# Performance work log

Hardware: AMD Instinct MI355X
Metric: run time of the kernel (lower is better)

Reference implementation:

```python
import jax, jax.numpy as jnp
import numpy as np

T, B, S, D, L, V = 32, 64, 64, 1024, 2, 32000


def _lstm_layer(x, h0, c0, wih, whh, bih, bhh):
    # x: (T, B, D_in); pytorch gate order: i, f, g, o
    b = bih + bhh
    xg = jnp.einsum('tbd,gd->tbg', x, wih) + b  # (T, B, 4D) precomputed input gates

    def step(carry, xg_t):
        h, c = carry
        gates = xg_t + h @ whh.T
        i, f, g, o = jnp.split(gates, 4, axis=-1)
        i, f, o = jax.nn.sigmoid(i), jax.nn.sigmoid(f), jax.nn.sigmoid(o)
        c = f * c + i * jnp.tanh(g)
        h = o * jnp.tanh(c)
        return (h, c), h

    (hT, cT), ys = jax.lax.scan(step, (h0, c0), xg)
    return ys, hT, cT


def setup_inputs() -> dict:
    key = jax.random.key(0)
    ks = jax.random.split(key, 20)
    s = 1.0 / np.sqrt(D)
    inp = {
        'input': jax.random.randint(ks[0], (T, B), 0, V),
        'h0': jax.random.normal(ks[1], (L, B, D)) * 0.1,
        'c0': jax.random.normal(ks[2], (L, B, D)) * 0.1,
        'context': jax.random.normal(ks[3], (S, B, D)) * 0.1,
        'init_output': jax.random.normal(ks[4], (B, D)) * 0.1,
        'emb_table': jax.random.normal(ks[5], (V, D)) * 0.02,
        'wih0': jax.random.normal(ks[6], (4 * D, D)) * s,
        'whh0': jax.random.normal(ks[7], (4 * D, D)) * s,
        'bih0': jax.random.normal(ks[8], (4 * D,)) * s,
        'bhh0': jax.random.normal(ks[9], (4 * D,)) * s,
        'wih1': jax.random.normal(ks[10], (4 * D, D)) * s,
        'whh1': jax.random.normal(ks[11], (4 * D, D)) * s,
        'bih1': jax.random.normal(ks[12], (4 * D,)) * s,
        'bhh1': jax.random.normal(ks[13], (4 * D,)) * s,
        'w_in': jax.random.normal(ks[14], (D, D)) * s,
        'w_out': jax.random.normal(ks[15], (D, 2 * D)) * s,
    }
    return inp


def reference(input, h0, c0, context, init_output, emb_table,
              wih0, whh0, bih0, bhh0, wih1, whh1, bih1, bhh1,
              w_in, w_out):
    # padding_idx=0 -> embedding row 0 is zero
    emb_table = emb_table.at[0].set(0.0)
    x = emb_table[input]  # (T, B, D)  (dropout=0 -> identity)

    layer_params = [(wih0, whh0, bih0, bhh0), (wih1, whh1, bih1, bhh1)]
    hs, cs = [], []
    for l in range(L):
        x, hT, cT = _lstm_layer(x, h0[l], c0[l], *layer_params[l])
        hs.append(hT)
        cs.append(cT)
    hn = jnp.stack(hs)  # (L, B, D)
    cn = jnp.stack(cs)

    # GlobalAttention over all timesteps at once (attn output never feeds back)
    ctx = jnp.transpose(context, (1, 0, 2))           # (B, S, D) == context.t()
    q = jnp.einsum('tbd,ed->tbe', x, w_in)            # linear_in(query)
    scores = jnp.einsum('tbd,bsd->tbs', q, ctx)       # (T, B, S)
    attn = jax.nn.softmax(scores, axis=-1)
    weighted = jnp.einsum('tbs,bsd->tbd', attn, ctx)  # (T, B, D)
    cat = jnp.concatenate([weighted, x], axis=-1)     # (T, B, 2D)
    out = jnp.tanh(jnp.einsum('tbe,de->tbd', cat, w_out))  # (T, B, D)

    return out, (hn, cn), attn[-1]
```

## Files before the change

### kernel.cpp

```cpp
#include <hip/hip_runtime.h>
#include <math.h>

#define T_ 32
#define B_ 64
#define S_ 64
#define D_ 1024

typedef __attribute__((ext_vector_type(8))) short short8;
typedef __attribute__((ext_vector_type(4))) float floatx4;

__device__ inline short8 ld8s(const short* p){ return *(const short8*)p; }
__device__ inline floatx4 mfma16(short8 a, short8 b, floatx4 c){
  return __builtin_amdgcn_mfma_f32_16x16x32_bf16(a, b, c, 0, 0, 0);
}
__device__ inline float sigm(float x){ return 1.0f/(1.0f+__expf(-x)); }

__device__ inline void load_lds16(const short* g, short* l){
  __builtin_amdgcn_global_load_lds(
      (const __attribute__((address_space(1))) unsigned int*)g,
      (__attribute__((address_space(3))) unsigned int*)l, 16, 0, 0);
}

__device__ inline short bfbits(float v){
  unsigned u = __builtin_bit_cast(unsigned, v);
  unsigned r = (u + 0x7FFFu + ((u >> 16) & 1u)) >> 16;
  return (short)r;
}
__device__ inline float bitsf(short s){
  unsigned u = ((unsigned)(unsigned short)s) << 16;
  return __builtin_bit_cast(float, u);
}
__device__ inline void split1(float v, short& h, short& l){
  h = bfbits(v); l = bfbits(v - bitsf(h));
}
__device__ inline void pack4(const float4& v, unsigned long long ws_unused,
                             uint2& hp, uint2& lp){
  short h0,h1,h2,h3,l0,l1,l2,l3;
  split1(v.x,h0,l0); split1(v.y,h1,l1); split1(v.z,h2,l2); split1(v.w,h3,l3);
  hp.x = (unsigned short)h0 | ((unsigned)(unsigned short)h1 << 16);
  hp.y = (unsigned short)h2 | ((unsigned)(unsigned short)h3 << 16);
  lp.x = (unsigned short)l0 | ((unsigned)(unsigned short)l1 << 16);
  lp.y = (unsigned short)l2 | ((unsigned)(unsigned short)l3 << 16);
}

__global__ __launch_bounds__(256) void split_kernel(const float* __restrict__ src,
                                                    short* __restrict__ hi,
                                                    short* __restrict__ lo){
  int i = blockIdx.x*256 + threadIdx.x;
  float4 v = ((const float4*)src)[i];
  uint2 hp, lp; pack4(v, 0, hp, lp);
  ((uint2*)hi)[i] = hp;
  ((uint2*)lo)[i] = lp;
}

__global__ __launch_bounds__(256) void split_whh(const float* __restrict__ src,
                                                 short* __restrict__ hi,
                                                 short* __restrict__ lo){
  int i = blockIdx.x*256 + threadIdx.x;
  int row = i >> 8, c4 = i & 255;
  int g = row >> 10, d = row & 1023;
  int nrow = ((d >> 2) << 4) + (g << 2) + (d & 3);
  float4 v = ((const float4*)src)[i];
  uint2 hp, lp; pack4(v, 0, hp, lp);
  int o = nrow*256 + c4;
  ((uint2*)hi)[o] = hp;
  ((uint2*)lo)[o] = lp;
}

__global__ __launch_bounds__(256) void embed_split(const int* __restrict__ tok,
                                                   const float* __restrict__ emb,
                                                   short* __restrict__ xh,
                                                   short* __restrict__ xl){
  int i = blockIdx.x*256 + threadIdx.x;
  int d4 = i & 255;
  int tb = i >> 8;
  int idx = tok[tb];
  float4 v;
  if (idx == 0) { v.x=v.y=v.z=v.w=0.f; }
  else          { v = ((const float4*)(emb + (size_t)idx*D_))[d4]; }
  uint2 hp, lp; pack4(v, 0, hp, lp);
  ((uint2*)xh)[i] = hp;
  ((uint2*)xl)[i] = lp;
}

__global__ __launch_bounds__(256) void init_state(const float* __restrict__ h0l,
                                                  const float* __restrict__ c0l,
                                                  short* __restrict__ hh, short* __restrict__ hl,
                                                  float* __restrict__ c){
  int i = blockIdx.x*256 + threadIdx.x;
  float4 v = ((const float4*)h0l)[i];
  uint2 hp, lp; pack4(v, 0, hp, lp);
  ((uint2*)hh)[i] = hp;
  ((uint2*)hl)[i] = lp;
  ((float4*)c)[i] = ((const float4*)c0l)[i];
}

__device__ inline void stage_tile(const short* __restrict__ G, int ld, int rowBase,
                                  int k0, short* lds, int wave, int lane){
#pragma unroll
  for (int c = 0; c < 2; ++c){
    int chunk = (wave*2 + c)*64 + lane;
    int row = chunk >> 2, kc = chunk & 3;
    const short* src = G + (size_t)(rowBase + row)*ld + k0 + kc*8;
    load_lds16(src, lds + (size_t)(wave*2 + c)*512);
  }
}

__global__ __launch_bounds__(256) void gemm128(
    const short* __restrict__ A1h, const short* __restrict__ A1l, int lda1,
    const short* __restrict__ B1h, const short* __restrict__ B1l, int ldb1, int K1,
    const short* __restrict__ A2h, const short* __restrict__ A2l, int lda2,
    const short* __restrict__ B2h, const short* __restrict__ B2l, int ldb2, int K2,
    const float* __restrict__ bias0, const float* __restrict__ bias1,
    float* __restrict__ Cf, short* __restrict__ Ch, short* __restrict__ Cl,
    int ldc, int act, int nbx)
{
  __shared__ short Ah[128*32];
  __shared__ short Al[128*32];
  __shared__ short Bh[128*32];
  __shared__ short Bl[128*32];

  const int nwg  = gridDim.x;
  const int w0   = blockIdx.x;
  const int wgid = (w0 & 7)*(nwg >> 3) + (w0 >> 3);
  const int bx = wgid % nbx, by = wgid / nbx;
  const int tid = threadIdx.x;
  const int wave = tid >> 6, lane = tid & 63;
  const int lr = lane & 15, qo = lane >> 4;
  const int wm = wave >> 1, wn = wave & 1;
  const int mBase = by*128, nBase = bx*128;

  floatx4 acc[4][4] = {};

  for (int pass = 0; pass < 2; ++pass){
    const short* pAh; const short* pAl; int lda;
    const short* pBh; const short* pBl; int ldb; int K;
    if (pass == 0){ pAh=A1h; pAl=A1l; lda=lda1; pBh=B1h; pBl=B1l; ldb=ldb1; K=K1; }
    else          { if (!A2h) break;
                    pAh=A2h; pAl=A2l; lda=lda2; pBh=B2h; pBl=B2l; ldb=ldb2; K=K2; }
    for (int k0 = 0; k0 < K; k0 += 32){
      stage_tile(pAh, lda, mBase, k0, Ah, wave, lane);
      stage_tile(pAl, lda, mBase, k0, Al, wave, lane);
      stage_tile(pBh, ldb, nBase, k0, Bh, wave, lane);
      stage_tile(pBl, ldb, nBase, k0, Bl, wave, lane);
      __syncthreads();
      short8 afh[4], afl[4], bfh[4], bfl[4];
#pragma unroll
      for (int f = 0; f < 4; ++f){
        int ar = wm*64 + f*16 + lr;
        int br = wn*64 + f*16 + lr;
        afh[f] = *(const short8*)&Ah[ar*32 + qo*8];
        afl[f] = *(const short8*)&Al[ar*32 + qo*8];
        bfh[f] = *(const short8*)&Bh[br*32 + qo*8];
        bfl[f] = *(const short8*)&Bl[br*32 + qo*8];
      }
#pragma unroll
      for (int mf = 0; mf < 4; ++mf)
#pragma unroll
        for (int nf = 0; nf < 4; ++nf){
          acc[mf][nf] = mfma16(afl[mf], bfh[nf], acc[mf][nf]);
          acc[mf][nf] = mfma16(afh[mf], bfl[nf], acc[mf][nf]);
          acc[mf][nf] = mfma16(afh[mf], bfh[nf], acc[mf][nf]);
        }
      __syncthreads();
    }
  }

  const int rb = qo*4;
#pragma unroll
  for (int nf = 0; nf < 4; ++nf){
    int col = nBase + wn*64 + nf*16 + lr;
    float badd = bias0 ? (bias0[col] + bias1[col]) : 0.f;
#pragma unroll
    for (int mf = 0; mf < 4; ++mf)
#pragma unroll
      for (int r = 0; r < 4; ++r){
        int row = mBase + wm*64 + mf*16 + rb + r;
        size_t idx = (size_t)row*ldc + col;
        float v = acc[mf][nf][r] + badd;
        if (act) v = tanhf(v);
        if (Cf) Cf[idx] = v;
        else { short h,l; split1(v,h,l); Ch[idx] = h; Cl[idx] = l; }
      }
  }
}

__global__ __launch_bounds__(512) void lstm_step3(
    const float* __restrict__ xg, int t,
    const short* __restrict__ whr_h, const short* __restrict__ whr_l,
    const short* __restrict__ hih, const short* __restrict__ hil,
    float* __restrict__ c,
    short* __restrict__ hoh, short* __restrict__ hol,
    short* __restrict__ xoh, short* __restrict__ xol,
    float* __restrict__ hn_out, float* __restrict__ cn_out)
{
  __shared__ short8 wv_h[16*128];
  __shared__ short8 wv_l[16*128];
  __shared__ float g_lds[2][64][17];
  const int j    = blockIdx.x;
  const int tid  = threadIdx.x;
  const int wave = tid >> 6;
  const int lane = tid & 63;
  const int lr   = lane & 15;
  const int qo   = lane >> 4;

  {
    const short8* srcH = (const short8*)(whr_h + (size_t)j*16*D_);
    const short8* srcL = (const short8*)(whr_l + (size_t)j*16*D_);
#pragma unroll
    for (int it = 0; it < 4; ++it) {
      int p = it*512 + tid;
      int row = p >> 7, pc = p & 127;
      int cc = pc ^ (row & 7);
      wv_h[p] = srcH[row*128 + cc];
      wv_l[p] = srcL[row*128 + cc];
    }
  }
  __syncthreads();

  const int bt = (wave & 3) * 16;
  const int kh = wave >> 2;
  const short8* ah8 = (const short8*)(hih + (size_t)(bt + lr)*D_);
  const short8* al8 = (const short8*)(hil + (size_t)(bt + lr)*D_);
  const int bswz = lr*128;
  const int bx   = lr & 7;
  floatx4 acc = {};
#pragma unroll 4
  for (int kc = kh*16; kc < kh*16 + 16; ++kc) {
    int cc = kc*4 + qo;
    short8 ahv = ah8[cc];
    short8 alv = al8[cc];
    int bi = bswz + (cc ^ bx);
    short8 bhv = wv_h[bi];
    short8 blv = wv_l[bi];
    acc = mfma16(alv, bhv, acc);
    acc = mfma16(ahv, blv, acc);
    acc = mfma16(ahv, bhv, acc);
  }
  int rb = qo*4;
#pragma unroll
  for (int r = 0; r < 4; ++r)
    g_lds[kh][bt + rb + r][lr] = acc[r];
  __syncthreads();

  if (tid < 256) {
    int b = tid >> 2, u = tid & 3;
    int d = j*4 + u;
    size_t xb = ((size_t)t*B_ + b)*(4*D_) + d;
    float i_ = sigm (g_lds[0][b][0*4+u] + g_lds[1][b][0*4+u] + xg[xb        ]);
    float f_ = sigm (g_lds[0][b][1*4+u] + g_lds[1][b][1*4+u] + xg[xb +   D_ ]);
    float gg = tanhf(g_lds[0][b][2*4+u] + g_lds[1][b][2*4+u] + xg[xb + 2*D_]);
    float o_ = sigm (g_lds[0][b][3*4+u] + g_lds[1][b][3*4+u] + xg[xb + 3*D_]);
    size_t ci = (size_t)b*D_ + d;
    float cn = f_*c[ci] + i_*gg;
    c[ci] = cn;
    float h = o_*tanhf(cn);
    short hh, hl; split1(h, hh, hl);
    hoh[ci] = hh; hol[ci] = hl;
    size_t xi = ((size_t)t*B_ + b)*D_ + d;
    xoh[xi] = hh; xol[xi] = hl;
    if (hn_out) { hn_out[ci] = h; cn_out[ci] = cn; }
  }
}

__global__ __launch_bounds__(256) void attn2(
    const short* __restrict__ qh, const short* __restrict__ ql,
    const short* __restrict__ cxh, const short* __restrict__ cxl,
    short* __restrict__ wth, short* __restrict__ wtl,
    float* __restrict__ attn_out)
{
  int b = blockIdx.x;
  __shared__ float sc[32][64];
  __shared__ short at_hi[32][64];
  __shared__ short at_lo[32][64];
  int wave = threadIdx.x >> 6;
  int lane = threadIdx.x & 63;
  int lr = lane & 15;
  int lk = (lane >> 4) * 8;
  int rb = (lane >> 4) * 4;

  {
    floatx4 acc[2] = {};
    int n0 = wave * 16;
    size_t Bo = ((size_t)(n0 + lr)*B_ + b)*D_ + lk;
    size_t A0 = ((size_t)(0  + lr)*B_ + b)*D_ + lk;
    size_t A1 = ((size_t)(16 + lr)*B_ + b)*D_ + lk;
    for (int k0 = 0; k0 < D_; k0 += 32) {
      short8 bh = ld8s(cxh + Bo + k0);
      short8 bl = ld8s(cxl + Bo + k0);
      short8 a0h = ld8s(qh + A0 + k0), a0l = ld8s(ql + A0 + k0);
      acc[0] = mfma16(a0l, bh, acc[0]);
      acc[0] = mfma16(a0h, bl, acc[0]);
      acc[0] = mfma16(a0h, bh, acc[0]);
      short8 a1h = ld8s(qh + A1 + k0), a1l = ld8s(ql + A1 + k0);
      acc[1] = mfma16(a1l, bh, acc[1]);
      acc[1] = mfma16(a1h, bl, acc[1]);
      acc[1] = mfma16(a1h, bh, acc[1]);
    }
#pragma unroll
    for (int m = 0; m < 2; ++m)
#pragma unroll
      for (int r = 0; r < 4; ++r)
        sc[m*16 + rb + r][n0 + lr] = acc[m][r];
  }
  __syncthreads();

  if (threadIdx.x < 32) {
    int t = threadIdx.x;
    float mx = -1e30f;
    for (int s = 0; s < 64; ++s) mx = fmaxf(mx, sc[t][s]);
    float sum = 0.f;
    for (int s = 0; s < 64; ++s) { float v = __expf(sc[t][s] - mx); sum += v; sc[t][s] = v; }
    float inv = 1.f / sum;
    for (int s = 0; s < 64; ++s) {
      float v = sc[t][s] * inv;
      short h, l; split1(v, h, l);
      at_hi[t][s] = h; at_lo[t][s] = l;
      if (t == 31) attn_out[b*64 + s] = v;
    }
  }
  __syncthreads();

  for (int i = 0; i < 16; ++i) {
    int n0 = (wave + 4*i) * 16;
    floatx4 acc[2] = {};
#pragma unroll
    for (int kk = 0; kk < 2; ++kk) {
      short8 bh, bl;
#pragma unroll
      for (int j = 0; j < 8; ++j) {
        int s = kk*32 + (lane >> 4)*8 + j;
        size_t o = ((size_t)s*B_ + b)*D_ + n0 + lr;
        bh[j] = cxh[o];
        bl[j] = cxl[o];
      }
      short8 a0h = *(const short8*)&at_hi[0  + lr][kk*32 + lk];
      short8 a0l = *(const short8*)&at_lo[0  + lr][kk*32 + lk];
      short8 a1h = *(const short8*)&at_hi[16 + lr][kk*32 + lk];
      short8 a1l = *(const short8*)&at_lo[16 + lr][kk*32 + lk];
      acc[0] = mfma16(a0l, bh, acc[0]);
      acc[0] = mfma16(a0h, bl, acc[0]);
      acc[0] = mfma16(a0h, bh, acc[0]);
      acc[1] = mfma16(a1l, bh, acc[1]);
      acc[1] = mfma16(a1h, bl, acc[1]);
      acc[1] = mfma16(a1h, bh, acc[1]);
    }
#pragma unroll
    for (int m = 0; m < 2; ++m)
#pragma unroll
      for (int r = 0; r < 4; ++r) {
        int t = m*16 + rb + r;
        size_t oi = ((size_t)t*B_ + b)*D_ + n0 + lr;
        float v = acc[m][r];
        short h, l; split1(v, h, l);
        wth[oi] = h; wtl[oi] = l;
      }
  }
}

extern "C" void kernel_launch(void* const* d_in, const int* in_sizes, int n_in,
                              void* d_out, int out_size, void* d_ws, size_t ws_size,
                              hipStream_t stream) {
  const int*   tok   = (const int*)  d_in[0];
  const float* h0    = (const float*)d_in[1];
  const float* c0    = (const float*)d_in[2];
  const float* ctx   = (const float*)d_in[3];
  const float* emb   = (const float*)d_in[5];
  const float* wih[2] = {(const float*)d_in[6],  (const float*)d_in[10]};
  const float* whh[2] = {(const float*)d_in[7],  (const float*)d_in[11]};
  const float* bih[2] = {(const float*)d_in[8],  (const float*)d_in[12]};
  const float* bhh[2] = {(const float*)d_in[9],  (const float*)d_in[13]};
  const float* w_in  = (const float*)d_in[14];
  const float* w_out = (const float*)d_in[15];
  float* outp = (float*)d_out;

  char* ws = (char*)d_ws;
#define MB(x) ((size_t)(x) << 20)
  short* x0h = (short*)(ws + MB(0));
  short* x0l = (short*)(ws + MB(4));
  short* x1h = (short*)(ws + MB(8));
  short* x1l = (short*)(ws + MB(12));
  short* x2h = (short*)(ws + MB(16));
  short* x2l = (short*)(ws + MB(20));
  float* xg  = (float*)(ws + MB(24));
  short* wihh = (short*)(ws + MB(56));
  short* wihl = (short*)(ws + MB(64));
  short* whhh = (short*)(ws + MB(72));
  short* whhl = (short*)(ws + MB(80));
  short* q_h  = x0h;
  short* q_l  = x0l;
  short* wt_h = x1h;
  short* wt_l = x1l;
  short* winh = (short*)(ws + MB(56));
  short* winl = (short*)(ws + MB(58));
  short* wouth = (short*)(ws + MB(60));
  short* woutl = (short*)(ws + MB(64));
  short* cxh = (short*)(ws + MB(72));
  short* cxl = (short*)(ws + MB(80));
  float* cbuf = (float*)(ws + MB(88));
  short* hbh  = (short*)(ws + MB(88) + 262144);
  short* hbl  = (short*)(ws + MB(88) + 524288);
#undef MB

  const size_t BD = (size_t)B_*D_;
  const size_t OUT_HN   = (size_t)T_*B_*D_;
  const size_t OUT_CN   = OUT_HN + 2*BD;
  const size_t OUT_ATTN = OUT_CN + 2*BD;

  embed_split<<<2048, 256, 0, stream>>>(tok, emb, x0h, x0l);

  for (int l = 0; l < 2; ++l) {
    const short* xinh = l ? x1h : x0h;
    const short* xinl = l ? x1l : x0l;
    short* xoh = l ? x2h : x1h;
    short* xol = l ? x2l : x1l;
    split_kernel<<<4096, 256, 0, stream>>>(wih[l], wihh, wihl);
    gemm128<<<512, 256, 0, stream>>>(
        xinh, xinl, D_, wihh, wihl, D_, D_,
        nullptr, nullptr, 0, nullptr, nullptr, 0, 0,
        bih[l], bhh[l], xg, nullptr, nullptr, 4*D_, 0, 32);
    split_whh<<<4096, 256, 0, stream>>>(whh[l], whhh, whhl);
    init_state<<<64, 256, 0, stream>>>(h0 + (size_t)l*BD, c0 + (size_t)l*BD,
                                       hbh, hbl, cbuf);
    for (int t = 0; t < T_; ++t) {
      bool last = (t == T_-1);
      lstm_step3<<<256, 512, 0, stream>>>(
          xg, t, whhh, whhl,
          hbh + (size_t)(t & 1)*BD,     hbl + (size_t)(t & 1)*BD,     cbuf,
          hbh + (size_t)((t+1) & 1)*BD, hbl + (size_t)((t+1) & 1)*BD,
          xoh, xol,
          last ? outp + OUT_HN + (size_t)l*BD : nullptr,
          last ? outp + OUT_CN + (size_t)l*BD : nullptr);
    }
  }

  split_kernel<<<1024, 256, 0, stream>>>(w_in,  winh,  winl);
  split_kernel<<<2048, 256, 0, stream>>>(w_out, wouth, woutl);
  gemm128<<<128, 256, 0, stream>>>(
      x2h, x2l, D_, winh, winl, D_, D_,
      nullptr, nullptr, 0, nullptr, nullptr, 0, 0,
      nullptr, nullptr, nullptr, q_h, q_l, D_, 0, 8);
  split_kernel<<<4096, 256, 0, stream>>>(ctx, cxh, cxl);
  attn2<<<64, 256, 0, stream>>>(q_h, q_l, cxh, cxl, wt_h, wt_l, outp + OUT_ATTN);
  gemm128<<<128, 256, 0, stream>>>(
      wt_h, wt_l, D_, wouth, woutl, 2*D_, D_,
      x2h, x2l, D_, wouth + D_, woutl + D_, 2*D_, D_,
      nullptr, nullptr, outp, nullptr, nullptr, D_, 1, 8);
}
```

Before: 1.404 ms.

## Fuse LSTM timesteps into persistent cooperative kernel with grid barriers

Replaces the 32 per-timestep lstm_step3 launches per layer with one cooperative persistent kernel. It loads the recurrent weight slice into LDS once, keeps the cell state in registers, and synchronizes all 256 blocks between steps with an atomic counter barrier. This removes per-step launch overhead and the repeated LDS weight reload and cell-state global traffic. The cost is a spin-wait grid barrier that needs all blocks co-resident, plus global-memory fence latency on each step.

Measured after the change: 2.368 ms. +68.7%, slower.

```diff
diff --git a/kernel.cpp b/kernel.cpp
--- a/kernel.cpp
+++ b/kernel.cpp
@@ -1,4 +1,5 @@
 #include <hip/hip_runtime.h>
+#include <hip/hip_cooperative_groups.h>
 #include <math.h>
 
 #define T_ 32
@@ -84,15 +85,13 @@
 }
 
 __global__ __launch_bounds__(256) void init_state(const float* __restrict__ h0l,
-                                                  const float* __restrict__ c0l,
-                                                  short* __restrict__ hh, short* __restrict__ hl,
-                                                  float* __restrict__ c){
+                                                  short* __restrict__ hh,
+                                                  short* __restrict__ hl){
   int i = blockIdx.x*256 + threadIdx.x;
   float4 v = ((const float4*)h0l)[i];
   uint2 hp, lp; pack4(v, 0, hp, lp);
   ((uint2*)hh)[i] = hp;
   ((uint2*)hl)[i] = lp;
-  ((float4*)c)[i] = ((const float4*)c0l)[i];
 }
 
 __device__ inline void stage_tile(const short* __restrict__ G, int ld, int rowBase,
@@ -185,14 +184,14 @@
   }
 }
 
-__global__ __launch_bounds__(512) void lstm_step3(
-    const float* __restrict__ xg, int t,
+__global__ __launch_bounds__(512) void lstm_persist(
+    const float* __restrict__ xg,
     const short* __restrict__ whr_h, const short* __restrict__ whr_l,
-    const short* __restrict__ hih, const short* __restrict__ hil,
-    float* __restrict__ c,
-    short* __restrict__ hoh, short* __restrict__ hol,
+    short* __restrict__ hbh, short* __restrict__ hbl,
+    const float* __restrict__ c0l,
     short* __restrict__ xoh, short* __restrict__ xol,
-    float* __restrict__ hn_out, float* __restrict__ cn_out)
+    float* __restrict__ hn_out, float* __restrict__ cn_out,
+    unsigned* __restrict__ cnt)
 {
   __shared__ short8 wv_h[16*128];
   __shared__ short8 wv_l[16*128];
@@ -216,50 +215,70 @@
       wv_l[p] = srcL[row*128 + cc];
     }
   }
+  const int b = tid >> 2, u = tid & 3;
+  const int d = j*4 + u;
+  float creg = 0.f;
+  if (tid < 256) creg = c0l[(size_t)b*D_ + d];
   __syncthreads();
 
   const int bt = (wave & 3) * 16;
   const int kh = wave >> 2;
-  const short8* ah8 = (const short8*)(hih + (size_t)(bt + lr)*D_);
-  const short8* al8 = (const short8*)(hil + (size_t)(bt + lr)*D_);
   const int bswz = lr*128;
-  const int bx   = lr & 7;
-  floatx4 acc = {};
+  const int bxr  = lr & 7;
+  const int rb = qo*4;
+
+  for (int t = 0; t < T_; ++t) {
+    const short* hih = hbh + (size_t)(t & 1)*(B_*D_);
+    const short* hil = hbl + (size_t)(t & 1)*(B_*D_);
+    const short8* ah8 = (const short8*)(hih + (size_t)(bt + lr)*D_);
+    const short8* al8 = (const short8*)(hil + (size_t)(bt + lr)*D_);
+    floatx4 acc = {};
 #pragma unroll 4
-  for (int kc = kh*16; kc < kh*16 + 16; ++kc) {
-    int cc = kc*4 + qo;
-    short8 ahv = ah8[cc];
-    short8 alv = al8[cc];
-    int bi = bswz + (cc ^ bx);
-    short8 bhv = wv_h[bi];
-    short8 blv = wv_l[bi];
-    acc = mfma16(alv, bhv, acc);
-    acc = mfma16(ahv, blv, acc);
-    acc = mfma16(ahv, bhv, acc);
-  }
-  int rb = qo*4;
-#pragma unroll
-  for (int r = 0; r < 4; ++r)
-    g_lds[kh][bt + rb + r][lr] = acc[r];
-  __syncthreads();
-
-  if (tid < 256) {
-    int b = tid >> 2, u = tid & 3;
-    int d = j*4 + u;
-    size_t xb = ((size_t)t*B_ + b)*(4*D_) + d;
-    float i_ = sigm (g_lds[0][b][0*4+u] + g_lds[1][b][0*4+u] + xg[xb        ]);
-    float f_ = sigm (g_lds[0][b][1*4+u] + g_lds[1][b][1*4+u] + xg[xb +   D_ ]);
-    float gg = tanhf(g_lds[0][b][2*4+u] + g_lds[1][b][2*4+u] + xg[xb + 2*D_]);
-    float o_ = sigm (g_lds[0][b][3*4+u] + g_lds[1][b][3*4+u] + xg[xb + 3*D_]);
-    size_t ci = (size_t)b*D_ + d;
-    float cn = f_*c[ci] + i_*gg;
-    c[ci] = cn;
-    float h = o_*tanhf(cn);
-    short hh, hl; split1(h, hh, hl);
-    hoh[ci] = hh; hol[ci] = hl;
-    size_t xi = ((size_t)t*B_ + b)*D_ + d;
-    xoh[xi] = hh; xol[xi] = hl;
-    if (hn_out) { hn_out[ci] = h; cn_out[ci] = cn; }
+    for (int kc = kh*16; kc < kh*16 + 16; ++kc) {
+      int cc = kc*4 + qo;
+      short8 ahv = ah8[cc];
+      short8 alv = al8[cc];
+      int bi = bswz + (cc ^ bxr);
+      short8 bhv = wv_h[bi];
+      short8 blv = wv_l[bi];
+      acc = mfma16(alv, bhv, acc);
+      acc = mfma16(ahv, blv, acc);
+      acc = mfma16(ahv, bhv, acc);
+    }
+#pragma unroll
+    for (int r = 0; r < 4; ++r)
+      g_lds[kh][bt + rb + r][lr] = acc[r];
+    __syncthreads();
+
+    if (tid < 256) {
+      size_t xb = ((size_t)t*B_ + b)*(4*D_) + d;
+      float i_ = sigm (g_lds[0][b][0*4+u] + g_lds[1][b][0*4+u] + xg[xb        ]);
+      float f_ = sigm (g_lds[0][b][1*4+u] + g_lds[1][b][1*4+u] + xg[xb +   D_ ]);
+      float gg = tanhf(g_lds[0][b][2*4+u] + g_lds[1][b][2*4+u] + xg[xb + 2*D_]);
+      float o_ = sigm (g_lds[0][b][3*4+u] + g_lds[1][b][3*4+u] + xg[xb + 3*D_]);
+      creg = f_*creg + i_*gg;
+      float h = o_*tanhf(creg);
+      short hh, hl; split1(h, hh, hl);
+      size_t ci = (size_t)b*D_ + d;
+      short* nh = hbh + (size_t)((t+1) & 1)*(B_*D_);
+      short* nl = hbl + (size_t)((t+1) & 1)*(B_*D_);
+      nh[ci] = hh; nl[ci] = hl;
+      size_t xi = ((size_t)t*B_ + b)*D_ + d;
+      xoh[xi] = hh; xol[xi] = hl;
+      if (t == T_-1) { hn_out[ci] = h; cn_out[ci] = creg; }
+    }
+    __syncthreads();
+
+    if (t < T_-1) {
+      if (tid == 0) {
+        __builtin_amdgcn_fence(__ATOMIC_RELEASE, "agent");
+        __hip_atomic_fetch_add(&cnt[t], 1u, __ATOMIC_RELAXED, __HIP_MEMORY_SCOPE_AGENT);
+        while (__hip_atomic_load(&cnt[t], __ATOMIC_RELAXED, __HIP_MEMORY_SCOPE_AGENT) < 256u)
+          __builtin_amdgcn_s_sleep(2);
+        __builtin_amdgcn_fence(__ATOMIC_ACQUIRE, "agent");
+      }
+      __syncthreads();
+    }
   }
 }
 
@@ -397,7 +416,7 @@
   short* woutl = (short*)(ws + MB(64));
   short* cxh = (short*)(ws + MB(72));
   short* cxl = (short*)(ws + MB(80));
-  float* cbuf = (float*)(ws + MB(88));
+  unsigned* cnt = (unsigned*)(ws + MB(88));
   short* hbh  = (short*)(ws + MB(88) + 262144);
   short* hbl  = (short*)(ws + MB(88) + 524288);
 #undef MB
@@ -407,6 +426,7 @@
   const size_t OUT_CN   = OUT_HN + 2*BD;
   const size_t OUT_ATTN = OUT_CN + 2*BD;
 
+  (void)hipMemsetAsync(cnt, 0, 64*sizeof(unsigned), stream);
   embed_split<<<2048, 256, 0, stream>>>(tok, emb, x0h, x0l);
 
   for (int l = 0; l < 2; ++l) {
@@ -420,17 +440,26 @@
         nullptr, nullptr, 0, nullptr, nullptr, 0, 0,
         bih[l], bhh[l], xg, nullptr, nullptr, 4*D_, 0, 32);
     split_whh<<<4096, 256, 0, stream>>>(whh[l], whhh, whhl);
-    init_state<<<64, 256, 0, stream>>>(h0 + (size_t)l*BD, c0 + (size_t)l*BD,
-                                       hbh, hbl, cbuf);
-    for (int t = 0; t < T_; ++t) {
-      bool last = (t == T_-1);
-      lstm_step3<<<256, 512, 0, stream>>>(
-          xg, t, whhh, whhl,
-          hbh + (size_t)(t & 1)*BD,     hbl + (size_t)(t & 1)*BD,     cbuf,
-          hbh + (size_t)((t+1) & 1)*BD, hbl + (size_t)((t+1) & 1)*BD,
-          xoh, xol,
-          last ? outp + OUT_HN + (size_t)l*BD : nullptr,
-          last ? outp + OUT_CN + (size_t)l*BD : nullptr);
+    init_state<<<64, 256, 0, stream>>>(h0 + (size_t)l*BD, hbh, hbl);
+    {
+      const float* xg_p = xg;
+      const short* whhh_c = whhh;
+      const short* whhl_c = whhl;
+      short* hbh_p = hbh;
+      short* hbl_p = hbl;
+      const float* c0l = c0 + (size_t)l*BD;
+      short* xoh_p = xoh;
+      short* xol_p = xol;
+      float* hn = outp + OUT_HN + (size_t)l*BD;
+      float* cn = outp + OUT_CN + (size_t)l*BD;
+      unsigned* cnt_l = cnt + l*32;
+      void* kargs[] = {
+        (void*)&xg_p, (void*)&whhh_c, (void*)&whhl_c,
+        (void*)&hbh_p, (void*)&hbl_p, (void*)&c0l,
+        (void*)&xoh_p, (void*)&xol_p, (void*)&hn, (void*)&cn, (void*)&cnt_l
+      };
+      (void)hipLaunchCooperativeKernel((const void*)lstm_persist, dim3(256), dim3(512),
+                                       kargs, 0, stream);
     }
   }
 
```
